# Optimization experiments

Hardware: AMD Instinct MI355X
Metric: run time of the kernel (lower is better)

## Reference

```python
import jax, jax.numpy as jnp
import numpy as np

BATCH = 32
NUM_VARS = 16
SAMPLES = 4096
EMBED_DIM = 128
WINDOW_SIZE = 32
STEP_SIZE = 4
WIDTH = 1.0


def setup_inputs() -> dict:
    key = jax.random.key(0)
    k1, k2, k3, k4, k5 = jax.random.split(key, 5)
    x = jax.random.normal(k1, (BATCH, NUM_VARS, SAMPLES), dtype=jnp.float32)
    # sample-level LSH: num_variables -> embed_dim
    W_sample = jax.random.normal(k2, (NUM_VARS, EMBED_DIM), dtype=jnp.float32)
    b_sample = jax.random.uniform(k3, (EMBED_DIM,), dtype=jnp.float32, minval=0.0, maxval=WIDTH)
    # patch-level LSH: window_size*embed_dim -> embed_dim
    W_patch = jax.random.normal(k4, (WINDOW_SIZE * EMBED_DIM, EMBED_DIM), dtype=jnp.float32)
    b_patch = jax.random.uniform(k5, (EMBED_DIM,), dtype=jnp.float32, minval=0.0, maxval=WIDTH)
    return {"x": x, "W_sample": W_sample, "b_sample": b_sample,
            "W_patch": W_patch, "b_patch": b_patch}


def reference(x, W_sample, b_sample, W_patch, b_patch):
    batch, v, samples = x.shape
    # encode: E2LSH hash of every timestep, fully vectorized over the samples axis
    # enc: [B, S, D]
    enc = jnp.floor((jnp.einsum('bvs,vd->bsd', x, W_sample) + b_sample) / WIDTH)
    # quantize: sliding windows over time, flattened then hashed
    num_tokens = (samples - WINDOW_SIZE) // STEP_SIZE  # matches preallocated tokens
    # idx: [T, W] gather indices for all windows at once
    idx = jnp.arange(num_tokens)[:, None] * STEP_SIZE + jnp.arange(WINDOW_SIZE)[None, :]
    windows = enc[:, idx, :].reshape(batch, num_tokens, WINDOW_SIZE * EMBED_DIM)  # [B, T, W*D]
    tokens = jnp.floor((windows @ W_patch + b_patch) / WIDTH)  # [B, T, D]
    return tokens
```

## Files before the change

kernel.cpp:

```cpp
#include <hip/hip_runtime.h>
#include <hip/hip_bf16.h>
#include <cstdint>

#define BATCH   32
#define NVARS   16
#define SAMPLES 4096
#define EDIM    128
#define NTOK    1016
#define PLELEM  4368

typedef __bf16 bf8_t __attribute__((ext_vector_type(8)));
typedef float  f4_t  __attribute__((ext_vector_type(4)));

__global__ __launch_bounds__(256) void prep_kernel(
    const float* __restrict__ Wp, __hip_bfloat16* __restrict__ WtF)
{
  __shared__ float ls[32][132];
  int tid = threadIdx.x;
  int kb  = blockIdx.x;
  int s = kb >> 3, dlt = kb & 7;
  int kbase = (4 * dlt + (s & 3)) * 128 + (s >> 2) * 32;
#pragma unroll
  for (int r = 0; r < 16; ++r) {
    int idx = tid + r * 256;
    ls[idx >> 7][idx & 127] =
        Wp[(size_t)(kbase + (idx >> 7)) * EDIM + (idx & 127)];
  }
  __syncthreads();
  int g = tid >> 5, l5 = tid & 31;
#pragma unroll
  for (int h = 0; h < 2; ++h) {
    int lane = l5 + h * 32;
    int quad = lane >> 4, l15 = lane & 15;
    int n = g * 16 + l15;
    union { unsigned short u[8]; uint4 v; } pk;
#pragma unroll
    for (int t = 0; t < 8; ++t) {
      __hip_bfloat16 hh = __float2bfloat16(ls[quad * 8 + t][n]);
      pk.u[t] = *(unsigned short*)&hh;
    }
    *(uint4*)(WtF + (size_t)kb * 4096 + g * 512 + lane * 8) = pk.v;
  }
}

__global__ __launch_bounds__(512, 2) void fused_kernel(
    const float* __restrict__ x,
    const float* __restrict__ Ws,
    const float* __restrict__ bs,
    const __hip_bfloat16* __restrict__ WtF,
    const float* __restrict__ bp,
    float* __restrict__ out)
{
  __shared__ __align__(16) __hip_bfloat16 Apan[16 * PLELEM];
  __shared__ __align__(16) float xTp[2][136][16];

  int tid  = threadIdx.x;
  int lane = tid & 63;
  int wv   = tid >> 6;
  int g2   = wv >> 1;
  int nh   = wv & 1;
  int b    = blockIdx.x >> 3;
  int t0   = (blockIdx.x & 7) << 7;
  int quad = lane >> 4;
  int l15  = lane & 15;

  const __hip_bfloat16* bg = WtF + (size_t)(nh * 4) * 512 + lane * 8;

  int q4 = tid & 31;
  int eq = q4 >> 3;
  int cq = (q4 >> 1) & 3;
  int hq = q4 & 1;
  int r0 = tid >> 5;

  float w[NVARS][4];
  float bz[4];
  {
    int d0 = q4 * 4;
#pragma unroll
    for (int v = 0; v < NVARS; ++v)
      *(float4*)&w[v][0] = *(const float4*)(Ws + v * EDIM + d0);
    *(float4*)&bz[0] = *(const float4*)(bs + d0);
  }

  int vv = tid & 15, rr = tid >> 4;
  float4 xreg[5];
  {
    const float* xb = x + ((size_t)b * NVARS + vv) * SAMPLES;
#pragma unroll
    for (int j = 0; j < 4; ++j) {
      int s4 = (t0 + rr + 32 * j) * 4;
      xreg[j] = *(const float4*)(xb + s4);
    }
    if (tid < 128) {
      int s4 = (t0 + 128 + rr) * 4;
      if (s4 > SAMPLES - 4) s4 = SAMPLES - 4;
      xreg[4] = *(const float4*)(xb + s4);
    }
  }

  auto stageX = [&](int p, int buf) {
#pragma unroll
    for (int j = 0; j < 4; ++j) {
      float c = (p == 0) ? xreg[j].x : (p == 1) ? xreg[j].y
              : (p == 2) ? xreg[j].z : xreg[j].w;
      xTp[buf][rr + 32 * j][vv] = c;
    }
    if (tid < 128) {
      float c = (p == 0) ? xreg[4].x : (p == 1) ? xreg[4].y
              : (p == 2) ? xreg[4].z : xreg[4].w;
      xTp[buf][128 + rr][vv] = c;
    }
  };

  auto encTask = [&](int p, int buf, int r) {
    const float* xr = &xTp[buf][r][0];
    float xv[NVARS];
    *(float4*)&xv[0]  = *(const float4*)(xr + 0);
    *(float4*)&xv[4]  = *(const float4*)(xr + 4);
    *(float4*)&xv[8]  = *(const float4*)(xr + 8);
    *(float4*)&xv[12] = *(const float4*)(xr + 12);
    float a0 = bz[0], a1 = bz[1], a2 = bz[2], a3 = bz[3];
#pragma unroll
    for (int v = 0; v < NVARS; ++v) {
      a0 += xv[v] * w[v][0]; a1 += xv[v] * w[v][1];
      a2 += xv[v] * w[v][2]; a3 += xv[v] * w[v][3];
    }
    union { unsigned short us[4]; uint2 q; } pk;
    pk.us[0] = (unsigned short)(__float_as_uint(floorf(a0)) >> 16);
    pk.us[1] = (unsigned short)(__float_as_uint(floorf(a1)) >> 16);
    pk.us[2] = (unsigned short)(__float_as_uint(floorf(a2)) >> 16);
    pk.us[3] = (unsigned short)(__float_as_uint(floorf(a3)) >> 16);
    int phys = (cq + (r >> 1)) & 3;
    char* plbase = (char*)&Apan[(eq * 4 + p) * PLELEM];
    *(uint2*)(plbase + r * 64 + phys * 16 + hq * 8) = pk.q;
  };

  stageX(0, 0);
  __syncthreads();
#pragma unroll
  for (int p = 0; p < 4; ++p) {
    if (p < 3) stageX(p + 1, (p + 1) & 1);
    int buf = p & 1;
#pragma unroll
    for (int j = 0; j < 8; ++j) encTask(p, buf, r0 + 16 * j);
    if (tid < 256) encTask(p, buf, 128 + (tid >> 5));
    __syncthreads();
  }

  f4_t acc[8][4];
  f4_t zero = {0.f, 0.f, 0.f, 0.f};
#pragma unroll
  for (int i = 0; i < 8; ++i)
#pragma unroll
    for (int j = 0; j < 4; ++j) acc[i][j] = zero;

  auto loadB = [&](int kb, uint4* d) {
#pragma unroll
    for (int j = 0; j < 4; ++j)
      d[j] = *(const uint4*)(bg + (size_t)kb * 4096 + j * 512);
  };

  auto loadAF0 = [&](bf8_t* af, const bf8_t* pA, int dlt) {
    int swz = (quad + ((t0 + dlt + l15) >> 1)) & 3;
#pragma unroll
    for (int i = 0; i < 4; ++i)
      af[i] = pA[(dlt + i * 16 + l15) * 4 + swz];
  };
  auto loadAF1 = [&](bf8_t* af, const bf8_t* pA, int dlt) {
    int swz = (quad + ((t0 + dlt + l15) >> 1)) & 3;
#pragma unroll
    for (int i = 0; i < 4; ++i)
      af[i] = pA[(dlt + (i + 4) * 16 + l15) * 4 + swz];
  };

  auto mstepH = [&](const bf8_t* af, const uint4* bq_, int mibase) {
    __builtin_amdgcn_s_setprio(1);
#pragma unroll
    for (int mi = 0; mi < 4; ++mi)
#pragma unroll
      for (int ni = 0; ni < 4; ++ni)
        acc[mibase + mi][ni] = __builtin_amdgcn_mfma_f32_16x16x32_bf16(
            af[mi], __builtin_bit_cast(bf8_t, bq_[ni]),
            acc[mibase + mi][ni], 0, 0, 0);
    __builtin_amdgcn_s_setprio(0);
  };

  bf8_t af0[4], af1[4];
  uint4 bq[2][4];
  loadB(g2 * 32 + 0, bq[0]);
  loadB(g2 * 32 + 1, bq[1]);
  loadAF0(af0, (const bf8_t*)&Apan[(g2 * 4) * PLELEM], 0);

  for (int ss = 0; ss < 4; ++ss) {
    const bf8_t* pA  = (const bf8_t*)&Apan[(g2 * 4 + ss) * PLELEM];
    const bf8_t* pAn = (const bf8_t*)&Apan[(g2 * 4 + ss + 1) * PLELEM];
#pragma unroll
    for (int d = 0; d < 8; ++d) {
      int kl = ss * 8 + d;
      loadAF1(af1, pA, d);
      mstepH(af0, bq[d & 1], 0);
      if (d < 7)       loadAF0(af0, pA, d + 1);
      else if (ss < 3) loadAF0(af0, pAn, 0);
      mstepH(af1, bq[d & 1], 4);
      if (kl < 30) loadB(g2 * 32 + kl + 2, bq[d & 1]);
    }
  }

  float* rb2 = (float*)&Apan[0];
  float bias[4];
#pragma unroll
  for (int ni = 0; ni < 4; ++ni) bias[ni] = bp[(nh << 6) + ni * 16 + l15];

#pragma unroll
  for (int rd = 0; rd < 4; ++rd) {
    __syncthreads();
    if (g2 > 0) {
      int slot = ((g2 - 1) * 2 + nh) * 64 + lane;
#pragma unroll
      for (int mh = 0; mh < 2; ++mh) {
        int mi = rd * 2 + mh;
#pragma unroll
        for (int ni = 0; ni < 4; ++ni)
          *(f4_t*)&rb2[(size_t)(slot + mh * 384) * 20 + ni * 4] = acc[mi][ni];
      }
    }
    __syncthreads();
    if (g2 == 0) {
#pragma unroll
      for (int mh = 0; mh < 2; ++mh) {
        int mi = rd * 2 + mh;
        f4_t s0 = acc[mi][0], s1 = acc[mi][1];
        f4_t s2 = acc[mi][2], s3 = acc[mi][3];
#pragma unroll
        for (int q = 1; q < 4; ++q) {
          int sl = ((q - 1) * 2 + nh) * 64 + lane + mh * 384;
          s0 += *(const f4_t*)&rb2[(size_t)sl * 20 + 0];
          s1 += *(const f4_t*)&rb2[(size_t)sl * 20 + 4];
          s2 += *(const f4_t*)&rb2[(size_t)sl * 20 + 8];
          s3 += *(const f4_t*)&rb2[(size_t)sl * 20 + 12];
        }
        f4_t sv[4] = {s0, s1, s2, s3};
#pragma unroll
        for (int ni = 0; ni < 4; ++ni)
#pragma unroll
          for (int r = 0; r < 4; ++r) {
            int t = t0 + mi * 16 + quad * 4 + r;
            if (t < NTOK) {
              int n = (nh << 6) + ni * 16 + l15;
              out[((size_t)b * NTOK + t) * EDIM + n] =
                  floorf(sv[ni][r] + bias[ni]);
            }
          }
      }
    }
  }
}

extern "C" void kernel_launch(void* const* d_in, const int* in_sizes, int n_in,
                              void* d_out, int out_size, void* d_ws, size_t ws_size,
                              hipStream_t stream) {
  const float* x  = (const float*)d_in[0];
  const float* Ws = (const float*)d_in[1];
  const float* bs = (const float*)d_in[2];
  const float* Wp = (const float*)d_in[3];
  const float* bp = (const float*)d_in[4];
  float* out = (float*)d_out;

  __hip_bfloat16* WtF = (__hip_bfloat16*)d_ws;

  prep_kernel<<<128, 256, 0, stream>>>(Wp, WtF);
  fused_kernel<<<BATCH * 8, 512, 0, stream>>>(x, Ws, bs, WtF, bp, out);
}
```

Baseline: 107.0 us.

## Warp-specialize fused kernel: encoder waves overlap with MFMA GEMM waves per phase

Splits the 8 waves into 4 encoder waves and 4 GEMM waves. Encoder waves compute the sample hash for phase p while GEMM waves run the patch MFMA for phase p-1, so encoding overlaps the matrix work instead of running ahead of it. Each GEMM wave group now covers two K-slices per phase, which cuts the cross-wave reduction to a single pairwise sum. The costs are that only half the waves issue MFMAs, encoder waves reload W every phase and read x with scalar loads, and the last phase is serialized.

New measurement: 115.1 us. 7.5% more time.

```diff
diff --git a/kernel.cpp b/kernel.cpp
--- a/kernel.cpp
+++ b/kernel.cpp
@@ -57,58 +57,43 @@
   int tid  = threadIdx.x;
   int lane = tid & 63;
   int wv   = tid >> 6;
-  int g2   = wv >> 1;
-  int nh   = wv & 1;
+  bool isenc = (wv >= 4);
   int b    = blockIdx.x >> 3;
   int t0   = (blockIdx.x & 7) << 7;
   int quad = lane >> 4;
   int l15  = lane & 15;
 
+  int g  = wv >> 1;
+  int nh = wv & 1;
   const __hip_bfloat16* bg = WtF + (size_t)(nh * 4) * 512 + lane * 8;
 
-  int q4 = tid & 31;
-  int eq = q4 >> 3;
-  int cq = (q4 >> 1) & 3;
-  int hq = q4 & 1;
-  int r0 = tid >> 5;
-
-  float w[NVARS][4];
-  float bz[4];
-  {
+  int et = tid & 255;
+  int q4 = et & 31;
+  int eq = q4 >> 3, cq = (q4 >> 1) & 3, hq = q4 & 1;
+  int r0 = et >> 5;
+  int vv = et & 15, rr = et >> 4;
+
+  float w[NVARS][4], bz[4];
+  auto loadW = [&]() {
     int d0 = q4 * 4;
 #pragma unroll
     for (int v = 0; v < NVARS; ++v)
       *(float4*)&w[v][0] = *(const float4*)(Ws + v * EDIM + d0);
     *(float4*)&bz[0] = *(const float4*)(bs + d0);
-  }
-
-  int vv = tid & 15, rr = tid >> 4;
-  float4 xreg[5];
-  {
+  };
+
+  auto stageX = [&](int p, int buf) {
     const float* xb = x + ((size_t)b * NVARS + vv) * SAMPLES;
 #pragma unroll
-    for (int j = 0; j < 4; ++j) {
-      int s4 = (t0 + rr + 32 * j) * 4;
-      xreg[j] = *(const float4*)(xb + s4);
-    }
-    if (tid < 128) {
-      int s4 = (t0 + 128 + rr) * 4;
-      if (s4 > SAMPLES - 4) s4 = SAMPLES - 4;
-      xreg[4] = *(const float4*)(xb + s4);
-    }
-  }
-
-  auto stageX = [&](int p, int buf) {
-#pragma unroll
-    for (int j = 0; j < 4; ++j) {
-      float c = (p == 0) ? xreg[j].x : (p == 1) ? xreg[j].y
-              : (p == 2) ? xreg[j].z : xreg[j].w;
-      xTp[buf][rr + 32 * j][vv] = c;
-    }
-    if (tid < 128) {
-      float c = (p == 0) ? xreg[4].x : (p == 1) ? xreg[4].y
-              : (p == 2) ? xreg[4].z : xreg[4].w;
-      xTp[buf][128 + rr][vv] = c;
+    for (int j = 0; j < 8; ++j) {
+      int row = rr + 16 * j;
+      xTp[buf][row][vv] = xb[(t0 + row) * 4 + p];
+    }
+    if (et < 128) {
+      int row = 128 + rr;
+      int sidx = (t0 + row) * 4 + p;
+      if (sidx > SAMPLES - 1) sidx = SAMPLES - 1;
+      xTp[buf][row][vv] = xb[sidx];
     }
   };
 
@@ -135,31 +120,20 @@
     *(uint2*)(plbase + r * 64 + phys * 16 + hq * 8) = pk.q;
   };
 
-  stageX(0, 0);
-  __syncthreads();
-#pragma unroll
-  for (int p = 0; p < 4; ++p) {
-    if (p < 3) stageX(p + 1, (p + 1) & 1);
-    int buf = p & 1;
-#pragma unroll
-    for (int j = 0; j < 8; ++j) encTask(p, buf, r0 + 16 * j);
-    if (tid < 256) encTask(p, buf, 128 + (tid >> 5));
-    __syncthreads();
-  }
-
   f4_t acc[8][4];
-  f4_t zero = {0.f, 0.f, 0.f, 0.f};
-#pragma unroll
-  for (int i = 0; i < 8; ++i)
-#pragma unroll
-    for (int j = 0; j < 4; ++j) acc[i][j] = zero;
+  if (!isenc) {
+    f4_t zero = {0.f, 0.f, 0.f, 0.f};
+#pragma unroll
+    for (int i = 0; i < 8; ++i)
+#pragma unroll
+      for (int j = 0; j < 4; ++j) acc[i][j] = zero;
+  }
 
   auto loadB = [&](int kb, uint4* d) {
 #pragma unroll
     for (int j = 0; j < 4; ++j)
       d[j] = *(const uint4*)(bg + (size_t)kb * 4096 + j * 512);
   };
-
   auto loadAF0 = [&](bf8_t* af, const bf8_t* pA, int dlt) {
     int swz = (quad + ((t0 + dlt + l15) >> 1)) & 3;
 #pragma unroll
@@ -172,7 +146,6 @@
     for (int i = 0; i < 4; ++i)
       af[i] = pA[(dlt + (i + 4) * 16 + l15) * 4 + swz];
   };
-
   auto mstepH = [&](const bf8_t* af, const uint4* bq_, int mibase) {
     __builtin_amdgcn_s_setprio(1);
 #pragma unroll
@@ -185,73 +158,82 @@
     __builtin_amdgcn_s_setprio(0);
   };
 
-  bf8_t af0[4], af1[4];
-  uint4 bq[2][4];
-  loadB(g2 * 32 + 0, bq[0]);
-  loadB(g2 * 32 + 1, bq[1]);
-  loadAF0(af0, (const bf8_t*)&Apan[(g2 * 4) * PLELEM], 0);
-
-  for (int ss = 0; ss < 4; ++ss) {
-    const bf8_t* pA  = (const bf8_t*)&Apan[(g2 * 4 + ss) * PLELEM];
-    const bf8_t* pAn = (const bf8_t*)&Apan[(g2 * 4 + ss + 1) * PLELEM];
-#pragma unroll
-    for (int d = 0; d < 8; ++d) {
-      int kl = ss * 8 + d;
-      loadAF1(af1, pA, d);
-      mstepH(af0, bq[d & 1], 0);
-      if (d < 7)       loadAF0(af0, pA, d + 1);
-      else if (ss < 3) loadAF0(af0, pAn, 0);
-      mstepH(af1, bq[d & 1], 4);
-      if (kl < 30) loadB(g2 * 32 + kl + 2, bq[d & 1]);
-    }
-  }
-
-  float* rb2 = (float*)&Apan[0];
-  float bias[4];
-#pragma unroll
-  for (int ni = 0; ni < 4; ++ni) bias[ni] = bp[(nh << 6) + ni * 16 + l15];
-
-#pragma unroll
-  for (int rd = 0; rd < 4; ++rd) {
+  auto gemmSS = [&](int ss) {
+    const bf8_t* plA = (const bf8_t*)&Apan[((2 * g) * 4 + ss) * PLELEM];
+    const bf8_t* plB = (const bf8_t*)&Apan[((2 * g + 1) * 4 + ss) * PLELEM];
+    int kb0 = (8 * g + ss) * 8;
+    int kb1 = (8 * g + 4 + ss) * 8;
+    uint4 bq[2][4];
+    loadB(kb0 + 0, bq[0]);
+    loadB(kb0 + 1, bq[1]);
+    bf8_t af0[4], af1[4];
+    loadAF0(af0, plA, 0);
+#pragma unroll
+    for (int dd = 0; dd < 16; ++dd) {
+      const bf8_t* pc = (dd < 8) ? plA : plB;
+      int dlt = dd & 7;
+      loadAF1(af1, pc, dlt);
+      mstepH(af0, bq[dd & 1], 0);
+      if (dd < 15) {
+        const bf8_t* pn = (dd + 1 < 8) ? plA : plB;
+        loadAF0(af0, pn, (dd + 1) & 7);
+      }
+      mstepH(af1, bq[dd & 1], 4);
+      int nk = dd + 2;
+      if (nk < 16) loadB((nk < 8 ? kb0 : kb1) + (nk & 7), bq[dd & 1]);
+    }
+  };
+
+  if (isenc) stageX(0, 0);
+  __syncthreads();
+
+#pragma unroll
+  for (int p = 0; p < 4; ++p) {
+    if (isenc) {
+      if (p < 3) stageX(p + 1, (p + 1) & 1);
+      loadW();
+#pragma unroll
+      for (int j = 0; j < 17; ++j) encTask(p, p & 1, r0 + 8 * j);
+    } else if (p > 0) {
+      gemmSS(p - 1);
+    }
     __syncthreads();
-    if (g2 > 0) {
-      int slot = ((g2 - 1) * 2 + nh) * 64 + lane;
-#pragma unroll
-      for (int mh = 0; mh < 2; ++mh) {
-        int mi = rd * 2 + mh;
-#pragma unroll
-        for (int ni = 0; ni < 4; ++ni)
-          *(f4_t*)&rb2[(size_t)(slot + mh * 384) * 20 + ni * 4] = acc[mi][ni];
-      }
-    }
-    __syncthreads();
-    if (g2 == 0) {
-#pragma unroll
-      for (int mh = 0; mh < 2; ++mh) {
-        int mi = rd * 2 + mh;
-        f4_t s0 = acc[mi][0], s1 = acc[mi][1];
-        f4_t s2 = acc[mi][2], s3 = acc[mi][3];
-#pragma unroll
-        for (int q = 1; q < 4; ++q) {
-          int sl = ((q - 1) * 2 + nh) * 64 + lane + mh * 384;
-          s0 += *(const f4_t*)&rb2[(size_t)sl * 20 + 0];
-          s1 += *(const f4_t*)&rb2[(size_t)sl * 20 + 4];
-          s2 += *(const f4_t*)&rb2[(size_t)sl * 20 + 8];
-          s3 += *(const f4_t*)&rb2[(size_t)sl * 20 + 12];
+  }
+  if (!isenc) gemmSS(3);
+
+  float* rb = (float*)&Apan[0];
+  __syncthreads();
+  if (!isenc && g == 1) {
+#pragma unroll
+    for (int mi = 0; mi < 8; ++mi)
+#pragma unroll
+      for (int ni = 0; ni < 4; ++ni)
+        *(f4_t*)&rb[(size_t)(mi * 128 + nh * 64 + lane) * 20 + ni * 4] =
+            acc[mi][ni];
+  }
+  __syncthreads();
+  if (!isenc && g == 0) {
+    float bias[4];
+#pragma unroll
+    for (int ni = 0; ni < 4; ++ni) bias[ni] = bp[nh * 64 + ni * 16 + l15];
+#pragma unroll
+    for (int mi = 0; mi < 8; ++mi) {
+      f4_t sv[4];
+#pragma unroll
+      for (int ni = 0; ni < 4; ++ni)
+        sv[ni] = acc[mi][ni] +
+            *(const f4_t*)&rb[(size_t)(mi * 128 + nh * 64 + lane) * 20 + ni * 4];
+#pragma unroll
+      for (int ni = 0; ni < 4; ++ni)
+#pragma unroll
+        for (int r = 0; r < 4; ++r) {
+          int t = t0 + mi * 16 + quad * 4 + r;
+          if (t < NTOK) {
+            int n = nh * 64 + ni * 16 + l15;
+            out[((size_t)b * NTOK + t) * EDIM + n] =
+                floorf(sv[ni][r] + bias[ni]);
+          }
         }
-        f4_t sv[4] = {s0, s1, s2, s3};
-#pragma unroll
-        for (int ni = 0; ni < 4; ++ni)
-#pragma unroll
-          for (int r = 0; r < 4; ++r) {
-            int t = t0 + mi * 16 + quad * 4 + r;
-            if (t < NTOK) {
-              int n = (nh << 6) + ni * 16 + l15;
-              out[((size_t)b * NTOK + t) * EDIM + n] =
-                  floorf(sv[ni][r] + bias[ni]);
-            }
-          }
-      }
     }
   }
 }
```
